# Kernel optimization log

Hardware: AMD Instinct MI355X
Metric: run time of the kernel (lower is better)

## Reference

```python
import jax, jax.numpy as jnp
import numpy as np

NUM_ENT = 50000
DIM = 128
NUM_REL = 1000  # num_rel * 2 (inverse relations)
E = 300000
SLOPE = 0.2      # args.leaky_relu_w
BN_EPS = 1e-5


def _leaky(x):
    return jax.nn.leaky_relu(x, SLOPE)


def _l2norm(x):
    n = jnp.linalg.norm(x, axis=-1, keepdims=True)
    return x / jnp.maximum(n, 1e-12)


def _batchnorm(x):
    # BatchNorm1d, training mode, fresh gamma=1/beta=0
    m = x.mean(axis=0)
    v = x.var(axis=0)
    return (x - m) / jnp.sqrt(v + BN_EPS)


def _propagate(i, j, etype, rel, x, watt, aatt, gcn, norm, num_ent):
    # gather -> relation-aware transform (opn='mult') -> attention -> scatter-add
    trans = x[j] * rel[etype]                       # [E, D]
    comb = jnp.concatenate([x[i], trans], axis=1)   # [E, 2D]
    score = (_leaky(comb @ watt) @ aatt)[:, 0]      # [E]
    # scatter softmax of attention score over destination nodes
    m = jax.ops.segment_max(score, i, num_segments=num_ent)
    m = jnp.where(jnp.isfinite(m), m, 0.0)
    e = jnp.exp(score - m[i])
    s = jax.ops.segment_sum(e, i, num_segments=num_ent)
    alpha = e / (s[i] + 1e-16)
    msg = (trans @ gcn) * alpha[:, None]
    if norm is not None:
        msg = msg * norm[:, None]
    return jax.ops.segment_sum(msg, i, num_segments=num_ent)


def _conv(ent, rel_in, edge_index, edge_type, w1, w2, gcn, loop_rel, watt, aatt):
    # RelationalAwareLayer.forward
    num_ent = ent.shape[0]
    rel = jnp.concatenate([rel_in, loop_rel], axis=0)
    rel = _leaky(rel @ w1) @ w2
    row, col = edge_index[0], edge_index[1]
    deg = jax.ops.segment_sum(jnp.ones((row.shape[0],), jnp.float32), row, num_segments=num_ent)
    dinv = jnp.where(deg > 0, deg ** -0.5, 0.0)
    norm = dinv[row]
    msg_n = _propagate(row, col, edge_type, rel, ent, watt, aatt, gcn, norm, num_ent)
    idx = jnp.arange(num_ent)
    loop_t = jnp.full((num_ent,), rel.shape[0] - 1)
    msg_s = _propagate(idx, idx, loop_t, rel, ent, watt, aatt, gcn, None, num_ent)
    return jnp.tanh(_batchnorm((msg_n + msg_s) / 2.0))


def setup_inputs() -> dict:
    key = jax.random.key(0)
    ks = jax.random.split(key, 24)
    g = lambda k, s: jax.random.normal(k, s, dtype=jnp.float32) * 0.05
    return {
        'edge_index': jax.random.randint(ks[0], (2, E), 0, NUM_ENT),
        'edge_type': jax.random.randint(ks[1], (E,), 0, NUM_REL),
        'ent_info_att': g(ks[2], (NUM_ENT, DIM)),
        'ent_completion_att': g(ks[3], (NUM_ENT, DIM)),
        'rel_completion_att': g(ks[4], (NUM_REL, DIM)),
        'rel_info_att': g(ks[5], (NUM_REL, DIM)),
        'align_linear1_1': g(ks[6], (2 * DIM, DIM)),
        'align_linear1_2': g(ks[7], (DIM, DIM)),
        'align_linear2_1': g(ks[8], (2 * DIM, DIM)),
        'align_linear2_2': g(ks[9], (DIM, DIM)),
        'rel_linear11': g(ks[10], (DIM, DIM)),
        'rel_linear12': g(ks[11], (DIM, DIM)),
        'rel_linear11_align': g(ks[12], (DIM, DIM)),
        'rel_linear12_align': g(ks[13], (DIM, DIM)),
        'all_linear_comp': g(ks[14], (3 * DIM, DIM)),
        # stacked per-layer conv params: [conv1_align, conv1_completion, conv2_align]
        'conv_w1': g(ks[15], (3, DIM, DIM)),
        'conv_w2': g(ks[16], (3, DIM, DIM)),
        'conv_gcn': g(ks[17], (3, DIM, DIM)),
        'conv_loop': g(ks[18], (3, 1, DIM)),
        'conv_watt': g(ks[19], (3, 2 * DIM, DIM)),
        'conv_aatt': g(ks[20], (3, DIM, 1)),
    }


def reference(edge_index, edge_type, ent_info_att, ent_completion_att,
              rel_completion_att, rel_info_att,
              align_linear1_1, align_linear1_2, align_linear2_1, align_linear2_2,
              rel_linear11, rel_linear12, rel_linear11_align, rel_linear12_align,
              all_linear_comp, conv_w1, conv_w2, conv_gcn, conv_loop, conv_watt, conv_aatt):
    # forward_base with num_gcn_layer == 2, dropout rate 0 (identity)
    init_comp = _l2norm(ent_completion_att)
    e1 = _leaky(jnp.concatenate([init_comp, ent_info_att], axis=1) @ align_linear1_1) @ align_linear1_2
    ao1 = _conv(e1, rel_info_att, edge_index, edge_type,
                conv_w1[0], conv_w2[0], conv_gcn[0], conv_loop[0], conv_watt[0], conv_aatt[0])
    co1 = _conv(ent_completion_att, rel_completion_att, edge_index, edge_type,
                conv_w1[1], conv_w2[1], conv_gcn[1], conv_loop[1], conv_watt[1], conv_aatt[1])
    pos1n = _l2norm(co1)
    e2 = _leaky(jnp.concatenate([pos1n, ao1], axis=1) @ align_linear2_1) @ align_linear2_2
    pr1 = _leaky(rel_completion_att @ rel_linear11) @ rel_linear12
    ari = _leaky(rel_info_att @ rel_linear11_align) @ rel_linear12_align
    ao2 = _conv(e2, ari, edge_index, edge_type,
                conv_w1[2], conv_w2[2], conv_gcn[2], conv_loop[2], conv_watt[2], conv_aatt[2])
    out = jnp.concatenate([e1, ao1, ao2], axis=1) @ all_linear_comp
    return (out, co1, pr1)
```

## Files before the change

### kernel.cpp

```cpp
#include <hip/hip_runtime.h>
#include <hip/hip_bf16.h>
#include <math.h>

#define D 128
#define DD 16384
#define NEMAX 96
typedef unsigned short u16;
typedef __attribute__((ext_vector_type(8))) short short8v;
typedef __attribute__((ext_vector_type(4))) short short4v;
typedef __attribute__((ext_vector_type(4))) float f32x4;

__device__ __forceinline__ u16 f2s(float v){
    union { __hip_bfloat16 h; u16 u; } c; c.h = __float2bfloat16(v); return c.u;
}
__device__ __forceinline__ float s2f(u16 u){
    union { __hip_bfloat16 h; u16 u; } c; c.u = u; return __bfloat162float(c.h);
}
__device__ __forceinline__ float lrelu(float x){ return x > 0.f ? x : 0.2f*x; }

__global__ void k_prepz(int* __restrict__ zz, int zw, int* __restrict__ nstart,
                        int* __restrict__ nend, int nb){
    int i = blockIdx.x*blockDim.x + threadIdx.x;
    int stride = gridDim.x*blockDim.x;
    for (int k = i; k < zw; k += stride) zz[k] = 0;
    for (int k = i; k < nb; k += stride){ nstart[k] = 0x7fffffff; nend[k] = -1; }
}
__global__ void k_f2b4(const float* __restrict__ in, u16* __restrict__ out, int n4){
    for (int i = blockIdx.x*blockDim.x + threadIdx.x; i < n4; i += gridDim.x*blockDim.x){
        float4 a = ((const float4*)in)[i];
        short4v pk;
        pk[0] = (short)f2s(a.x); pk[1] = (short)f2s(a.y);
        pk[2] = (short)f2s(a.z); pk[3] = (short)f2s(a.w);
        *(short4v*)(out + (size_t)i*4) = pk;
    }
}
__global__ void k_ideg(const int* __restrict__ row, int* __restrict__ deg, int E_){
    for (int i = blockIdx.x*blockDim.x + threadIdx.x; i < E_; i += gridDim.x*blockDim.x)
        atomicAdd(&deg[row[i]], 1);
}
__global__ void k_scan1(const int* __restrict__ ideg, int* __restrict__ rowptr,
                        int* __restrict__ bsum, int n){
    __shared__ int buf[256];
    int t = threadIdx.x, i = blockIdx.x*256 + t;
    int v = (i < n) ? ideg[i] : 0;
    buf[t] = v;
    __syncthreads();
    #pragma unroll
    for (int o = 1; o < 256; o <<= 1){
        int u = (t >= o) ? buf[t-o] : 0;
        __syncthreads();
        buf[t] += u;
        __syncthreads();
    }
    if (i < n) rowptr[i] = buf[t] - v;
    if (t == 255) bsum[blockIdx.x] = buf[255];
}
__global__ void k_scan2(int* __restrict__ bsum, int nb){
    __shared__ int buf[256];
    __shared__ int carry_s;
    int t = threadIdx.x;
    if (t == 0) carry_s = 0;
    __syncthreads();
    for (int base = 0; base < nb; base += 256){
        int v = (base + t < nb) ? bsum[base + t] : 0;
        buf[t] = v;
        __syncthreads();
        #pragma unroll
        for (int o = 1; o < 256; o <<= 1){
            int u = (t >= o) ? buf[t-o] : 0;
            __syncthreads();
            buf[t] += u;
            __syncthreads();
        }
        if (base + t < nb) bsum[base + t] = carry_s + buf[t] - v;
        int last = buf[255];
        __syncthreads();
        if (t == 0) carry_s += last;
        __syncthreads();
    }
}
__global__ void k_scan3(int* __restrict__ rowptr, const int* __restrict__ bsum,
                        int n, int E_){
    int i = blockIdx.x*blockDim.x + threadIdx.x;
    if (i < n) rowptr[i] += bsum[i >> 8];
    if (i == 0) rowptr[n] = E_;
}
__global__ void k_scatter(const int* __restrict__ row, const int* __restrict__ rowptr,
                          int* __restrict__ cnt, int* __restrict__ perm, int E_){
    for (int e = blockIdx.x*blockDim.x + threadIdx.x; e < E_; e += gridDim.x*blockDim.x){
        int i = row[e];
        int pos = rowptr[i] + atomicAdd(&cnt[i], 1);
        perm[pos] = e;
    }
}
__global__ void k_bmap(const int* __restrict__ rowptr, int* __restrict__ nstart,
                       int* __restrict__ nend, int n){
    for (int i = blockIdx.x*blockDim.x + threadIdx.x; i < n; i += gridDim.x*blockDim.x){
        int s = rowptr[i], e = rowptr[i+1];
        if (e > s){
            int b = s >> 6;
            atomicMin(&nstart[b], i);
            atomicMax(&nend[b], i);
        }
    }
}
__global__ void k_bnapply(const u16* __restrict__ acc, const float* __restrict__ gp,
                          float inv_ne, int n, u16* __restrict__ dstb,
                          float* __restrict__ dstf){
    int d = threadIdx.x & 127;
    float m = gp[d] * inv_ne;
    float var = gp[128 + d] * inv_ne - m*m;
    float sc = rsqrtf(var + 1e-5f);
    for (int i = blockIdx.x*blockDim.x + threadIdx.x; i < n; i += gridDim.x*blockDim.x){
        float v = s2f(acc[i]) * 0.5f;
        float r = tanhf((v - m) * sc);
        dstb[i] = f2s(r);
        if (dstf) dstf[i] = r;
    }
}
__global__ void k_bnapply2(const u16* __restrict__ acc0, const float* __restrict__ gp0,
                           u16* __restrict__ d0b,
                           const u16* __restrict__ acc1, const float* __restrict__ gp1,
                           u16* __restrict__ d1b, float* __restrict__ d1f,
                           float inv_ne, int n, int gb){
    int pb = blockIdx.x >= gb;
    const u16* acc = pb ? acc1 : acc0;
    const float* gp = pb ? gp1 : gp0;
    u16* db = pb ? d1b : d0b;
    float* df = pb ? d1f : nullptr;
    int b = blockIdx.x - (pb ? gb : 0);
    int d = threadIdx.x & 127;
    float m = gp[d] * inv_ne;
    float var = gp[128 + d] * inv_ne - m*m;
    float sc = rsqrtf(var + 1e-5f);
    for (int i = b*blockDim.x + threadIdx.x; i < n; i += gb*blockDim.x){
        float v = s2f(acc[i]) * 0.5f;
        float r = tanhf((v - m) * sc);
        db[i] = f2s(r);
        if (df) df[i] = r;
    }
}

__global__ void k_relprep(const float* __restrict__ rel_comp, const float* __restrict__ rel_info,
        const float* __restrict__ rl11, const float* __restrict__ rl12,
        const float* __restrict__ rl11a, const float* __restrict__ rl12a,
        const float* __restrict__ cloop, const float* __restrict__ cw1,
        const float* __restrict__ cw2, float* __restrict__ pr1out,
        float* __restrict__ rel2all, int NR){
    int b = blockIdx.x, t = threadIdx.x;
    __shared__ float v[D];
    __shared__ float h[D];
    if (b < NR){
        v[t] = rel_comp[(size_t)b*D + t];
        __syncthreads();
        float a = 0.f;
        #pragma unroll 8
        for (int k = 0; k < D; k++) a += v[k] * rl11[(size_t)k*D + t];
        h[t] = lrelu(a);
        __syncthreads();
        float o = 0.f;
        #pragma unroll 8
        for (int k = 0; k < D; k++) o += h[k] * rl12[(size_t)k*D + t];
        pr1out[(size_t)b*D + t] = o;
        return;
    }
    int bb = b - NR;
    int l = bb / (NR+1), r = bb - l*(NR+1);
    float xv;
    if (r == NR)      xv = cloop[l*D + t];
    else if (l == 1)  xv = rel_comp[(size_t)r*D + t];
    else              xv = rel_info[(size_t)r*D + t];
    v[t] = xv;
    __syncthreads();
    if (l == 2 && r < NR){
        float a = 0.f;
        #pragma unroll 8
        for (int k = 0; k < D; k++) a += v[k] * rl11a[(size_t)k*D + t];
        h[t] = lrelu(a);
        __syncthreads();
        float o = 0.f;
        #pragma unroll 8
        for (int k = 0; k < D; k++) o += h[k] * rl12a[(size_t)k*D + t];
        v[t] = o;
        __syncthreads();
    }
    const float* w1 = cw1 + (size_t)l*DD;
    const float* w2 = cw2 + (size_t)l*DD;
    float a = 0.f;
    #pragma unroll 8
    for (int k = 0; k < D; k++) a += v[k] * w1[(size_t)k*D + t];
    h[t] = lrelu(a);
    __syncthreads();
    float o = 0.f;
    #pragma unroll 8
    for (int k = 0; k < D; k++) o += h[k] * w2[(size_t)k*D + t];
    rel2all[((size_t)l*(NR+1) + r)*D + t] = o;
}

struct TEnt { const float* s; u16* d; int ldd; };
struct TTab { TEnt e[18]; };
__global__ void k_wprep(TTab tab){
    TEnt en = tab.e[blockIdx.x];
    int t = threadIdx.x;
    int n = t >> 1, h = t & 1;
    #pragma unroll
    for (int g = 0; g < 8; ++g){
        int k0 = h*64 + g*8;
        short8v pk;
        #pragma unroll
        for (int q = 0; q < 8; ++q) pk[q] = (short)f2s(en.s[(size_t)(k0+q)*D + n]);
        *(short8v*)(en.d + (size_t)n*en.ldd + k0) = pk;
    }
}

struct Srcs { const void* p0; const void* p1; const void* p2; int f0, f1, f2; };

template<int NSEG, int EPI, bool RSN>
__global__ __launch_bounds__(256) void k_mrow(Srcs S, const u16* __restrict__ WT,
        void* __restrict__ out, int NE_){
    __shared__ __align__(16) short As[128*128];
    int tid = threadIdx.x;
    int row0 = blockIdx.x * 128;
    int lane = tid & 63, w = tid >> 6;
    int l15 = lane & 15, lq = lane >> 4;
    int nhalf = w & 1, mquad = w >> 1;
    f32x4 acc[4][4];
    #pragma unroll
    for (int a = 0; a < 4; a++)
        #pragma unroll
        for (int b = 0; b < 4; b++) acc[a][b] = (f32x4){0.f,0.f,0.f,0.f};

    int sr = tid >> 1, sh = tid & 1;
    int rr = row0 + sr; if (rr >= NE_) rr = NE_ - 1;

    #pragma unroll
    for (int s = 0; s < NSEG; ++s){
        const void* sp = (s == 0) ? S.p0 : (s == 1) ? S.p1 : S.p2;
        int sf = (s == 0) ? S.f0 : (s == 1) ? S.f1 : S.f2;
        if (s) __syncthreads();
        #pragma unroll
        for (int g = 0; g < 8; ++g){
            int k8 = sh*64 + g*8;
            short8v pk;
            if (sf){
                const float* fp = (const float*)sp + (size_t)rr*D + k8;
                #pragma unroll
                for (int q = 0; q < 8; ++q) pk[q] = (short)f2s(fp[q]);
            } else {
                pk = *(const short8v*)((const u16*)sp + (size_t)rr*D + k8);
            }
            *(short8v*)(As + sr*D + (((k8>>3) ^ (sr&7))<<3)) = pk;
        }
        if (RSN && s == 0){
            float ss = 0.f;
            #pragma unroll
            for (int g = 0; g < 8; ++g){
                int k8 = sh*64 + g*8;
                short8v v = *(const short8v*)(As + sr*D + (((k8>>3) ^ (sr&7))<<3));
                #pragma unroll
                for (int q = 0; q < 8; ++q){ float f = s2f((u16)v[q]); ss += f*f; }
            }
            ss += __shfl_xor(ss, 1, 64);
            float rsc = 1.f / fmaxf(sqrtf(ss), 1e-12f);
            #pragma unroll
            for (int g = 0; g < 8; ++g){
                int k8 = sh*64 + g*8;
                short* ap = As + sr*D + (((k8>>3) ^ (sr&7))<<3);
                short8v v = *(const short8v*)ap;
                short8v pk;
                #pragma unroll
                for (int q = 0; q < 8; ++q) pk[q] = (short)f2s(s2f((u16)v[q]) * rsc);
                *(short8v*)ap = pk;
            }
        }
        __syncthreads();
        short8v bfr[4][4];
        #pragma unroll
        for (int nt = 0; nt < 4; ++nt)
            #pragma unroll
            for (int kk = 0; kk < 4; ++kk){
                size_t idx = (size_t)(nhalf*64 + nt*16 + l15)*(NSEG*D) + (size_t)s*D + kk*32 + lq*8;
                bfr[nt][kk] = *(const short8v*)(WT + idx);
            }
        #pragma unroll
        for (int mt = 0; mt < 4; ++mt){
            int ar = mquad*64 + mt*16 + l15;
            short8v afr[4];
            #pragma unroll
            for (int kk = 0; kk < 4; ++kk)
                afr[kk] = *(const short8v*)(As + ar*D + (((kk*4 + lq) ^ (ar&7))<<3));
            #pragma unroll
            for (int nt = 0; nt < 4; ++nt)
                #pragma unroll
                for (int kk = 0; kk < 4; ++kk)
                    acc[mt][nt] = __builtin_amdgcn_mfma_f32_16x16x32_bf16(
                        afr[kk], bfr[nt][kk], acc[mt][nt], 0, 0, 0);
        }
    }
    #pragma unroll
    for (int mt = 0; mt < 4; ++mt){
        #pragma unroll
        for (int nt = 0; nt < 4; ++nt){
            #pragma unroll
            for (int r = 0; r < 4; ++r){
                int gr = row0 + mquad*64 + mt*16 + lq*4 + r;
                if (gr >= NE_) continue;
                int c = nhalf*64 + nt*16 + l15;
                float v = acc[mt][nt][r];
                if (EPI == 0) ((float*)out)[(size_t)gr*D + c] = v;
                else ((u16*)out)[(size_t)gr*D + c] = f2s(EPI == 2 ? lrelu(v) : v);
            }
        }
    }
}

struct ConvP { const u16* x; const u16* WT; u16* out; u16* ub; const float* loop; float* gp; };

template<int MODE>
__global__ __launch_bounds__(256) void k_mrow2(ConvP A, ConvP B, int rb, int NE_){
    __shared__ __align__(16) short As[128*128];
    int pb = blockIdx.x >= rb;
    ConvP P = pb ? B : A;
    int row0 = (blockIdx.x - (pb ? rb : 0)) * 128;
    int tid = threadIdx.x;
    int lane = tid & 63, w = tid >> 6;
    int l15 = lane & 15, lq = lane >> 4;
    int nhalf = w & 1, mquad = w >> 1;
    f32x4 acc[4][4];
    #pragma unroll
    for (int a = 0; a < 4; a++)
        #pragma unroll
        for (int b = 0; b < 4; b++) acc[a][b] = (f32x4){0.f,0.f,0.f,0.f};

    int sr = tid >> 1, sh = tid & 1;
    int rr = row0 + sr; if (rr >= NE_) rr = NE_ - 1;
    #pragma unroll
    for (int g = 0; g < 8; ++g){
        int k8 = sh*64 + g*8;
        short8v pk = *(const short8v*)(P.x + (size_t)rr*D + k8);
        *(short8v*)(As + sr*D + (((k8>>3) ^ (sr&7))<<3)) = pk;
    }
    __syncthreads();
    short8v bfr[4][4];
    #pragma unroll
    for (int nt = 0; nt < 4; ++nt)
        #pragma unroll
        for (int kk = 0; kk < 4; ++kk)
            bfr[nt][kk] = *(const short8v*)(P.WT + (size_t)(nhalf*64 + nt*16 + l15)*D + kk*32 + lq*8);
    #pragma unroll
    for (int mt = 0; mt < 4; ++mt){
        int ar = mquad*64 + mt*16 + l15;
        short8v afr[4];
        #pragma unroll
        for (int kk = 0; kk < 4; ++kk)
            afr[kk] = *(const short8v*)(As + ar*D + (((kk*4 + lq) ^ (ar&7))<<3));
        #pragma unroll
        for (int nt = 0; nt < 4; ++nt)
            #pragma unroll
            for (int kk = 0; kk < 4; ++kk)
                acc[mt][nt] = __builtin_amdgcn_mfma_f32_16x16x32_bf16(
                    afr[kk], bfr[nt][kk], acc[mt][nt], 0, 0, 0);
    }
    if (MODE == 3){
        float cs[4] = {0,0,0,0}, cs2[4] = {0,0,0,0};
        #pragma unroll
        for (int mt = 0; mt < 4; ++mt)
            #pragma unroll
            for (int nt = 0; nt < 4; ++nt)
                #pragma unroll
                for (int r = 0; r < 4; ++r){
                    int gr = row0 + mquad*64 + mt*16 + lq*4 + r;
                    if (gr >= NE_) continue;
                    int c = nhalf*64 + nt*16 + l15;
                    float v = acc[mt][nt][r];
                    P.out[(size_t)gr*D + c] = f2s(v);
                    float h = v * 0.5f;
                    cs[nt] += h; cs2[nt] += h*h;
                }
        __syncthreads();
        float* ps  = (float*)As;
        float* ps2 = ps + 1024;
        int slot = mquad*4 + lq;
        #pragma unroll
        for (int nt = 0; nt < 4; ++nt){
            int c = nhalf*64 + nt*16 + l15;
            ps[slot*128 + c]  = cs[nt];
            ps2[slot*128 + c] = cs2[nt];
        }
        __syncthreads();
        if (tid < 128){
            float s = 0.f, s2 = 0.f;
            #pragma unroll
            for (int q = 0; q < 8; ++q){ s += ps[q*128 + tid]; s2 += ps2[q*128 + tid]; }
            atomicAdd(&P.gp[tid], s);
            atomicAdd(&P.gp[128 + tid], s2);
        }
    } else {
        #pragma unroll
        for (int mt = 0; mt < 4; ++mt)
            #pragma unroll
            for (int nt = 0; nt < 4; ++nt)
                #pragma unroll
                for (int r = 0; r < 4; ++r){
                    int gr = row0 + mquad*64 + mt*16 + lq*4 + r;
                    if (gr >= NE_) continue;
                    int c = nhalf*64 + nt*16 + l15;
                    P.out[(size_t)gr*D + c] = f2s(acc[mt][nt][r]);
                }
        for (int idx = tid; idx < 128*128; idx += 256){
            int r2 = idx >> 7, c = idx & 127;
            int gr = row0 + r2;
            if (gr < NE_){
                float v = s2f((u16)As[r2*D + ((((c>>3) ^ (r2&7))<<3) | (c&7))]) * P.loop[c];
                P.ub[(size_t)gr*D + c] = f2s(v);
            }
        }
    }
}

struct FP { const u16* x; const float* rel2; const u16* xattb; const u16* WT;
            const float* aatt; const float* loop; u16* u; };

__global__ __launch_bounds__(256) void k_fedge(
        const int* __restrict__ coli, const int* __restrict__ ety,
        const int* __restrict__ rowptr, const int* __restrict__ perm,
        const int* __restrict__ nstart, const int* __restrict__ nend,
        FP fa, FP fb, int nb){
    __shared__ __align__(16) short As[NEMAX*D];
    __shared__ u16 jL[NEMAX], kL[NEMAX], iL[NEMAX];
    __shared__ float sc[NEMAX];
    __shared__ float red[2][NEMAX];
    int pb = blockIdx.x >= nb;
    FP P = pb ? fb : fa;
    int b = blockIdx.x - (pb ? nb : 0);
    int ns = nstart[b];
    if (ns == 0x7fffffff) return;
    int nn = nend[b] - ns + 1;
    int tid = threadIdx.x;
    int estart = rowptr[ns];
    int ne = rowptr[ns + nn] - estart;
    if (ne > NEMAX) ne = NEMAX;
    int T = (ne + 15) >> 4;
    int nrows = T << 4;
    if (tid < ne){
        int e = perm[estart + tid];
        jL[tid] = (u16)coli[e]; kL[tid] = (u16)ety[e];
    }
    if (tid < nn){
        int i = ns + tid;
        int s0 = rowptr[i] - estart, s1 = rowptr[i+1] - estart;
        if (s0 < 0) s0 = 0;
        if (s1 > NEMAX) s1 = NEMAX;
        for (int p = s0; p < s1; ++p) iL[p] = (u16)i;
    }
    __syncthreads();
    for (int it = tid; it < nrows*4; it += 256){
        int p = it >> 2, part = it & 3;
        int ps = (p < ne) ? p : (ne - 1);
        int j = jL[ps], krel = kL[ps];
        #pragma unroll
        for (int g = 0; g < 4; ++g){
            int k8 = part*32 + g*8;
            short8v sv = *(const short8v*)(P.x + (size_t)j*D + k8);
            const float* rp = P.rel2 + (size_t)krel*D + k8;
            short8v pk;
            #pragma unroll
            for (int q = 0; q < 8; ++q) pk[q] = (short)f2s(s2f((u16)sv[q]) * rp[q]);
            *(short8v*)(As + p*D + (((k8>>3) ^ (p&7))<<3)) = pk;
        }
    }
    __syncthreads();
    int lane = tid & 63, w = tid >> 6;
    int l15 = lane & 15, lq = lane >> 4;
    int nhalf = w & 1, mq = w >> 1;
    short8v bfr[4][4];
    #pragma unroll
    for (int nt = 0; nt < 4; ++nt)
        #pragma unroll
        for (int kk = 0; kk < 4; ++kk)
            bfr[nt][kk] = *(const short8v*)(P.WT + (size_t)(nhalf*64 + nt*16 + l15)*D + kk*32 + lq*8);
    float av[4];
    #pragma unroll
    for (int nt = 0; nt < 4; ++nt) av[nt] = P.aatt[nhalf*64 + nt*16 + l15];

    for (int t = mq; t < T; t += 2){
        float xv[4][4];
        #pragma unroll
        for (int r = 0; r < 4; ++r){
            int el = t*16 + lq*4 + r;
            int ep = (el < ne) ? el : (ne - 1);
            int ii = iL[ep];
            #pragma unroll
            for (int nt = 0; nt < 4; ++nt)
                xv[r][nt] = s2f(P.xattb[(size_t)ii*D + nhalf*64 + nt*16 + l15]);
        }
        int ar = t*16 + l15;
        short8v afr[4];
        #pragma unroll
        for (int kk = 0; kk < 4; ++kk)
            afr[kk] = *(const short8v*)(As + ar*D + (((kk*4 + lq) ^ (ar&7))<<3));
        f32x4 acc[4];
        #pragma unroll
        for (int nt = 0; nt < 4; ++nt) acc[nt] = (f32x4){0.f,0.f,0.f,0.f};
        #pragma unroll
        for (int nt = 0; nt < 4; ++nt)
            #pragma unroll
            for (int kk = 0; kk < 4; ++kk)
                acc[nt] = __builtin_amdgcn_mfma_f32_16x16x32_bf16(
                    afr[kk], bfr[nt][kk], acc[nt], 0, 0, 0);
        #pragma unroll
        for (int r = 0; r < 4; ++r){
            int el = t*16 + lq*4 + r;
            float p = 0.f;
            if (el < ne){
                #pragma unroll
                for (int nt = 0; nt < 4; ++nt)
                    p += lrelu(acc[nt][r] + xv[r][nt]) * av[nt];
            }
            p += __shfl_xor(p, 1, 64);
            p += __shfl_xor(p, 2, 64);
            p += __shfl_xor(p, 4, 64);
            p += __shfl_xor(p, 8, 64);
            if (l15 == 0 && el < NEMAX) red[nhalf][el] = p;
        }
    }
    __syncthreads();
    if (tid < ne) sc[tid] = expf(red[0][tid] + red[1][tid]);
    __syncthreads();
    if (tid < nn){
        int i = ns + tid;
        int s0 = rowptr[i] - estart, s1 = rowptr[i+1] - estart;
        if (s1 > NEMAX) s1 = NEMAX;
        if (s1 > s0){
            float sum = 0.f;
            for (int p = s0; p < s1; ++p) sum += sc[p];
            float coef = rsqrtf((float)(s1 - s0)) / (sum + 1e-16f);
            for (int p = s0; p < s1; ++p) sc[p] *= coef;
        }
    }
    __syncthreads();
    int c = tid & 127, nh = tid >> 7;
    float loopc = P.loop[c];
    for (int n0 = nh; n0 < nn; n0 += 16){
        float xi[8];
        int cnt = 0;
        for (int n = n0; n < nn && cnt < 8; n += 2, ++cnt)
            xi[cnt] = s2f(P.x[(size_t)(ns + n)*D + c]);
        cnt = 0;
        for (int n = n0; n < nn && cnt < 8; n += 2, ++cnt){
            int i = ns + n;
            int s0 = rowptr[i] - estart, s1 = rowptr[i+1] - estart;
            if (s1 > NEMAX) s1 = NEMAX;
            if (s1 <= s0) continue;
            float a = xi[cnt] * loopc;
            int p = s0;
            for (; p + 4 <= s1; p += 4){
                float v0 = s2f((u16)As[(p+0)*D + ((((c>>3) ^ ((p+0)&7))<<3) | (c&7))]);
                float v1 = s2f((u16)As[(p+1)*D + ((((c>>3) ^ ((p+1)&7))<<3) | (c&7))]);
                float v2 = s2f((u16)As[(p+2)*D + ((((c>>3) ^ ((p+2)&7))<<3) | (c&7))]);
                float v3 = s2f((u16)As[(p+3)*D + ((((c>>3) ^ ((p+3)&7))<<3) | (c&7))]);
                a += sc[p]*v0 + sc[p+1]*v1 + sc[p+2]*v2 + sc[p+3]*v3;
            }
            for (; p < s1; ++p)
                a += sc[p] * s2f((u16)As[p*D + ((((c>>3) ^ (p&7))<<3) | (c&7))]);
            P.u[(size_t)i*D + c] = f2s(a);
        }
    }
}

extern "C" void kernel_launch(void* const* d_in, const int* in_sizes, int n_in,
                              void* d_out, int out_size, void* d_ws, size_t ws_size,
                              hipStream_t stream){
    const int* eidx = (const int*)d_in[0];
    const int* ety  = (const int*)d_in[1];
    const float* ent_info = (const float*)d_in[2];
    const float* ent_comp = (const float*)d_in[3];
    const float* rel_comp = (const float*)d_in[4];
    const float* rel_info = (const float*)d_in[5];
    const float* al11 = (const float*)d_in[6],  *al12 = (const float*)d_in[7];
    const float* al21 = (const float*)d_in[8],  *al22 = (const float*)d_in[9];
    const float* rl11 = (const float*)d_in[10], *rl12 = (const float*)d_in[11];
    const float* rl11a = (const float*)d_in[12], *rl12a = (const float*)d_in[13];
    const float* allw = (const float*)d_in[14];
    const float* cw1 = (const float*)d_in[15], *cw2 = (const float*)d_in[16];
    const float* cgcn = (const float*)d_in[17], *cloop = (const float*)d_in[18];
    const float* cwatt = (const float*)d_in[19], *caatt = (const float*)d_in[20];

    const int E  = in_sizes[1];
    const int NE = in_sizes[2] / D;
    const int NR = in_sizes[4] / D;
    const int* row = eidx;
    const int* col = eidx + E;
    const size_t NEd = (size_t)NE * D;
    float* outp = (float*)d_out;
    const int NB64 = (E + 63) / 64;

    char* wsb = (char*)d_ws;
    size_t off = 0;
    auto takeB = [&](size_t bytes) -> void* {
        void* q = wsb + off;
        off = (off + bytes + 255) & ~(size_t)255;
        return q;
    };
    u16*   slotA = (u16*) takeB(NEd * 2);
    u16*   hb    = slotA;
    u16*   accB0 = slotA;
    u16*   xattb0= (u16*) takeB(NEd * 2);
    u16*   ub0   = (u16*) takeB(NEd * 2);
    u16*   e1b   = (u16*) takeB(NEd * 2);
    u16*   ao1b  = (u16*) takeB(NEd * 2);
    u16*   e2b   = (u16*) takeB(NEd * 2);
    u16*   cob   = (u16*) takeB(NEd * 2);
    float* rel2all = (float*)takeB((size_t)3*(NR+1)*D*4);
    int*   rowptr= (int*)  takeB((size_t)(NE+1)*4);
    int*   perm  = (int*)  takeB((size_t)E*4);
    int*   bsum  = (int*)  takeB(1024*4);
    int*   nstart= (int*)  takeB((size_t)NB64*4);
    int*   nend  = (int*)  takeB((size_t)NB64*4);
    int ZW = 2*NE + 768;
    int*   zz    = (int*)  takeB((size_t)ZW*4);
    int*   ideg  = zz;
    int*   cnt   = zz + NE;
    float* gp3   = (float*)(zz + 2*NE);
    u16*   wtXatt = (u16*)takeB((size_t)3*DD*2);
    u16*   wtScore= (u16*)takeB((size_t)3*DD*2);
    u16*   wtGcn  = (u16*)takeB((size_t)3*DD*2);
    u16*   wtAl11 = (u16*)takeB((size_t)2*DD*2);
    u16*   wtAl12 = (u16*)takeB((size_t)DD*2);
    u16*   wtAl21 = (u16*)takeB((size_t)2*DD*2);
    u16*   wtAl22 = (u16*)takeB((size_t)DD*2);
    u16*   wtAllw = (u16*)takeB((size_t)3*DD*2);
    u16*   xcb   = e2b;

    size_t slab = ((NEd*2 + 255) & ~(size_t)255);
    bool wide = (off + 3*slab) <= ws_size;
    u16* xattb1 = wide ? (u16*)takeB(NEd * 2) : xattb0;
    u16* ub1    = wide ? (u16*)takeB(NEd * 2) : ub0;
    u16* accB1  = wide ? (u16*)takeB(NEd * 2) : accB0;

    const int GS = 2048, BS = 256;
    const int RB = (NE + 127) / 128;
    const int NB = (NE + 255) / 256;
    const float inv_ne = 1.f / (float)NE;

    TTab tab;
    int ti = 0;
    for (int l = 0; l < 3; ++l){
        tab.e[ti++] = { cwatt + (size_t)l*2*DD,        wtXatt  + (size_t)l*DD, 128 };
        tab.e[ti++] = { cwatt + (size_t)l*2*DD + DD,   wtScore + (size_t)l*DD, 128 };
        tab.e[ti++] = { cgcn  + (size_t)l*DD,          wtGcn   + (size_t)l*DD, 128 };
    }
    tab.e[ti++] = { al11,       wtAl11,        256 };
    tab.e[ti++] = { al11 + DD,  wtAl11 + 128,  256 };
    tab.e[ti++] = { al12,       wtAl12,        128 };
    tab.e[ti++] = { al21,       wtAl21,        256 };
    tab.e[ti++] = { al21 + DD,  wtAl21 + 128,  256 };
    tab.e[ti++] = { al22,       wtAl22,        128 };
    tab.e[ti++] = { allw,            wtAllw,        384 };
    tab.e[ti++] = { allw + DD,       wtAllw + 128,  384 };
    tab.e[ti++] = { allw + 2*DD,     wtAllw + 256,  384 };
    k_wprep<<<18, 256, 0, stream>>>(tab);

    k_prepz<<<256, BS, 0, stream>>>(zz, ZW, nstart, nend, NB64);
    k_f2b4<<<GS, BS, 0, stream>>>(ent_comp, xcb, (int)(NEd/4));
    k_ideg<<<GS, BS, 0, stream>>>(row, ideg, E);
    k_scan1<<<NB, 256, 0, stream>>>(ideg, rowptr, bsum, NE);
    k_scan2<<<1, 256, 0, stream>>>(bsum, NB);
    k_scan3<<<NB, 256, 0, stream>>>(rowptr, bsum, NE, E);
    k_scatter<<<GS, BS, 0, stream>>>(row, rowptr, cnt, perm, E);
    k_bmap<<<NB, 256, 0, stream>>>(rowptr, nstart, nend, NE);

    k_relprep<<<NR + 3*(NR+1), D, 0, stream>>>(rel_comp, rel_info, rl11, rl12,
                                               rl11a, rl12a, cloop, cw1, cw2,
                                               outp + 2*NEd, rel2all, NR);

    {
        Srcs S{ ent_comp, ent_info, nullptr, 1, 1, 0 };
        k_mrow<2, 2, true><<<RB, 256, 0, stream>>>(S, wtAl11, hb, NE);
        Srcs S2{ hb, nullptr, nullptr, 0, 0, 0 };
        k_mrow<1, 1, false><<<RB, 256, 0, stream>>>(S2, wtAl12, e1b, NE);
    }

    auto conv_seq = [&](const u16* x, int l, u16* xab, u16* ubp, u16* acb,
                        u16* dstb, float* dstf){
        const float* rel2l = rel2all + (size_t)l*(NR+1)*D;
        float* gp = gp3 + (size_t)l*256;
        ConvP A4{ x, wtXatt + (size_t)l*DD, xab, ubp, rel2l + (size_t)NR*D, nullptr };
        k_mrow2<4><<<RB, 256, 0, stream>>>(A4, A4, RB, NE);
        FP fa{ x, rel2l, xab, wtScore + (size_t)l*DD, caatt + (size_t)l*D,
               rel2l + (size_t)NR*D, ubp };
        k_fedge<<<NB64, 256, 0, stream>>>(col, ety, rowptr, perm, nstart, nend,
                                          fa, fa, NB64);
        ConvP A3{ ubp, wtGcn + (size_t)l*DD, acb, nullptr, nullptr, gp };
        k_mrow2<3><<<RB, 256, 0, stream>>>(A3, A3, RB, NE);
        k_bnapply<<<GS, BS, 0, stream>>>(acb, gp, inv_ne, (int)NEd, dstb, dstf);
    };

    if (wide){
        const float* rel2_0 = rel2all;
        const float* rel2_1 = rel2all + (size_t)(NR+1)*D;
        ConvP A4{ e1b, wtXatt,      xattb0, ub0, rel2_0 + (size_t)NR*D, nullptr };
        ConvP B4{ xcb, wtXatt + DD, xattb1, ub1, rel2_1 + (size_t)NR*D, nullptr };
        k_mrow2<4><<<2*RB, 256, 0, stream>>>(A4, B4, RB, NE);
        FP fa{ e1b, rel2_0, xattb0, wtScore,      caatt,     rel2_0 + (size_t)NR*D, ub0 };
        FP fb{ xcb, rel2_1, xattb1, wtScore + DD, caatt + D, rel2_1 + (size_t)NR*D, ub1 };
        k_fedge<<<2*NB64, 256, 0, stream>>>(col, ety, rowptr, perm, nstart, nend,
                                            fa, fb, NB64);
        ConvP A3{ ub0, wtGcn,      accB0, nullptr, nullptr, gp3 };
        ConvP B3{ ub1, wtGcn + DD, accB1, nullptr, nullptr, gp3 + 256 };
        k_mrow2<3><<<2*RB, 256, 0, stream>>>(A3, B3, RB, NE);
        k_bnapply2<<<2*GS, BS, 0, stream>>>(accB0, gp3, ao1b,
                                            accB1, gp3 + 256, cob, outp + NEd,
                                            inv_ne, (int)NEd, GS);
    } else {
        conv_seq(e1b, 0, xattb0, ub0, accB0, ao1b, nullptr);
        conv_seq(xcb, 1, xattb0, ub0, accB0, cob, outp + NEd);
    }

    {
        Srcs S{ cob, ao1b, nullptr, 0, 0, 0 };
        k_mrow<2, 2, true><<<RB, 256, 0, stream>>>(S, wtAl21, hb, NE);
        Srcs S2{ hb, nullptr, nullptr, 0, 0, 0 };
        k_mrow<1, 1, false><<<RB, 256, 0, stream>>>(S2, wtAl22, e2b, NE);
    }

    conv_seq(e2b, 2, xattb0, ub0, accB0, cob, nullptr);

    {
        Srcs S{ e1b, ao1b, cob, 0, 0, 0 };
        k_mrow<3, 0, false><<<RB, 256, 0, stream>>>(S, wtAllw, outp, NE);
    }
}
```

Measured before the change: 685.7 us.

## Pack col/etype into sorted edge array and fold block map into scan

The scatter kernel now writes a packed (col, etype) word per sorted edge position instead of a permutation index, so the edge kernel reads one contiguous array rather than doing indirect gathers through perm into col and ety. The k_bmap kernel is removed and its node-to-block min/max bookkeeping moves into k_scan3 using ideg, which drops one launch. The final per-node aggregation loop in k_fedge is simplified by removing the x prefetch batching. Packing assumes col fits in 16 bits, which the earlier u16 casts already assumed.

```diff
diff --git a/kernel.cpp b/kernel.cpp
--- a/kernel.cpp
+++ b/kernel.cpp
@@ -80,28 +80,27 @@
     }
 }
 __global__ void k_scan3(int* __restrict__ rowptr, const int* __restrict__ bsum,
-                        int n, int E_){
+                        const int* __restrict__ ideg, int* __restrict__ nstart,
+                        int* __restrict__ nend, int n, int E_){
     int i = blockIdx.x*blockDim.x + threadIdx.x;
-    if (i < n) rowptr[i] += bsum[i >> 8];
-    if (i == 0) rowptr[n] = E_;
-}
-__global__ void k_scatter(const int* __restrict__ row, const int* __restrict__ rowptr,
-                          int* __restrict__ cnt, int* __restrict__ perm, int E_){
+    if (i < n){
+        int rpi = rowptr[i] + bsum[i >> 8];
+        rowptr[i] = rpi;
+        if (i == 0) rowptr[n] = E_;
+        if (ideg[i] > 0){
+            int b = rpi >> 6;
+            atomicMin(&nstart[b], i);
+            atomicMax(&nend[b], i);
+        }
+    }
+}
+__global__ void k_scatter(const int* __restrict__ row, const int* __restrict__ col,
+                          const int* __restrict__ ety, const int* __restrict__ rowptr,
+                          int* __restrict__ cnt, unsigned* __restrict__ jk, int E_){
     for (int e = blockIdx.x*blockDim.x + threadIdx.x; e < E_; e += gridDim.x*blockDim.x){
         int i = row[e];
         int pos = rowptr[i] + atomicAdd(&cnt[i], 1);
-        perm[pos] = e;
-    }
-}
-__global__ void k_bmap(const int* __restrict__ rowptr, int* __restrict__ nstart,
-                       int* __restrict__ nend, int n){
-    for (int i = blockIdx.x*blockDim.x + threadIdx.x; i < n; i += gridDim.x*blockDim.x){
-        int s = rowptr[i], e = rowptr[i+1];
-        if (e > s){
-            int b = s >> 6;
-            atomicMin(&nstart[b], i);
-            atomicMax(&nend[b], i);
-        }
+        jk[pos] = ((unsigned)col[e] & 0xFFFFu) | ((unsigned)ety[e] << 16);
     }
 }
 __global__ void k_bnapply(const u16* __restrict__ acc, const float* __restrict__ gp,
@@ -422,8 +421,8 @@
             const float* aatt; const float* loop; u16* u; };
 
 __global__ __launch_bounds__(256) void k_fedge(
-        const int* __restrict__ coli, const int* __restrict__ ety,
-        const int* __restrict__ rowptr, const int* __restrict__ perm,
+        const unsigned* __restrict__ jk,
+        const int* __restrict__ rowptr,
         const int* __restrict__ nstart, const int* __restrict__ nend,
         FP fa, FP fb, int nb){
     __shared__ __align__(16) short As[NEMAX*D];
@@ -443,8 +442,8 @@
     int T = (ne + 15) >> 4;
     int nrows = T << 4;
     if (tid < ne){
-        int e = perm[estart + tid];
-        jL[tid] = (u16)coli[e]; kL[tid] = (u16)ety[e];
+        unsigned v = jk[estart + tid];
+        jL[tid] = (u16)(v & 0xFFFFu); kL[tid] = (u16)(v >> 16);
     }
     if (tid < nn){
         int i = ns + tid;
@@ -541,30 +540,23 @@
     __syncthreads();
     int c = tid & 127, nh = tid >> 7;
     float loopc = P.loop[c];
-    for (int n0 = nh; n0 < nn; n0 += 16){
-        float xi[8];
-        int cnt = 0;
-        for (int n = n0; n < nn && cnt < 8; n += 2, ++cnt)
-            xi[cnt] = s2f(P.x[(size_t)(ns + n)*D + c]);
-        cnt = 0;
-        for (int n = n0; n < nn && cnt < 8; n += 2, ++cnt){
-            int i = ns + n;
-            int s0 = rowptr[i] - estart, s1 = rowptr[i+1] - estart;
-            if (s1 > NEMAX) s1 = NEMAX;
-            if (s1 <= s0) continue;
-            float a = xi[cnt] * loopc;
-            int p = s0;
-            for (; p + 4 <= s1; p += 4){
-                float v0 = s2f((u16)As[(p+0)*D + ((((c>>3) ^ ((p+0)&7))<<3) | (c&7))]);
-                float v1 = s2f((u16)As[(p+1)*D + ((((c>>3) ^ ((p+1)&7))<<3) | (c&7))]);
-                float v2 = s2f((u16)As[(p+2)*D + ((((c>>3) ^ ((p+2)&7))<<3) | (c&7))]);
-                float v3 = s2f((u16)As[(p+3)*D + ((((c>>3) ^ ((p+3)&7))<<3) | (c&7))]);
-                a += sc[p]*v0 + sc[p+1]*v1 + sc[p+2]*v2 + sc[p+3]*v3;
-            }
-            for (; p < s1; ++p)
-                a += sc[p] * s2f((u16)As[p*D + ((((c>>3) ^ (p&7))<<3) | (c&7))]);
-            P.u[(size_t)i*D + c] = f2s(a);
-        }
+    for (int n = nh; n < nn; n += 2){
+        int i = ns + n;
+        int s0 = rowptr[i] - estart, s1 = rowptr[i+1] - estart;
+        if (s1 > NEMAX) s1 = NEMAX;
+        if (s1 <= s0) continue;
+        float a = s2f(P.x[(size_t)i*D + c]) * loopc;
+        int p = s0;
+        for (; p + 4 <= s1; p += 4){
+            float v0 = s2f((u16)As[(p+0)*D + ((((c>>3) ^ ((p+0)&7))<<3) | (c&7))]);
+            float v1 = s2f((u16)As[(p+1)*D + ((((c>>3) ^ ((p+1)&7))<<3) | (c&7))]);
+            float v2 = s2f((u16)As[(p+2)*D + ((((c>>3) ^ ((p+2)&7))<<3) | (c&7))]);
+            float v3 = s2f((u16)As[(p+3)*D + ((((c>>3) ^ ((p+3)&7))<<3) | (c&7))]);
+            a += sc[p]*v0 + sc[p+1]*v1 + sc[p+2]*v2 + sc[p+3]*v3;
+        }
+        for (; p < s1; ++p)
+            a += sc[p] * s2f((u16)As[p*D + ((((c>>3) ^ (p&7))<<3) | (c&7))]);
+        P.u[(size_t)i*D + c] = f2s(a);
     }
 }
 
@@ -613,7 +605,7 @@
     u16*   cob   = (u16*) takeB(NEd * 2);
     float* rel2all = (float*)takeB((size_t)3*(NR+1)*D*4);
     int*   rowptr= (int*)  takeB((size_t)(NE+1)*4);
-    int*   perm  = (int*)  takeB((size_t)E*4);
+    unsigned* jk = (unsigned*)takeB((size_t)E*4);
     int*   bsum  = (int*)  takeB(1024*4);
     int*   nstart= (int*)  takeB((size_t)NB64*4);
     int*   nend  = (int*)  takeB((size_t)NB64*4);
@@ -666,9 +658,8 @@
     k_ideg<<<GS, BS, 0, stream>>>(row, ideg, E);
     k_scan1<<<NB, 256, 0, stream>>>(ideg, rowptr, bsum, NE);
     k_scan2<<<1, 256, 0, stream>>>(bsum, NB);
-    k_scan3<<<NB, 256, 0, stream>>>(rowptr, bsum, NE, E);
-    k_scatter<<<GS, BS, 0, stream>>>(row, rowptr, cnt, perm, E);
-    k_bmap<<<NB, 256, 0, stream>>>(rowptr, nstart, nend, NE);
+    k_scan3<<<NB, 256, 0, stream>>>(rowptr, bsum, ideg, nstart, nend, NE, E);
+    k_scatter<<<GS, BS, 0, stream>>>(row, col, ety, rowptr, cnt, jk, E);
 
     k_relprep<<<NR + 3*(NR+1), D, 0, stream>>>(rel_comp, rel_info, rl11, rl12,
                                                rl11a, rl12a, cloop, cw1, cw2,
@@ -689,8 +680,7 @@
         k_mrow2<4><<<RB, 256, 0, stream>>>(A4, A4, RB, NE);
         FP fa{ x, rel2l, xab, wtScore + (size_t)l*DD, caatt + (size_t)l*D,
                rel2l + (size_t)NR*D, ubp };
-        k_fedge<<<NB64, 256, 0, stream>>>(col, ety, rowptr, perm, nstart, nend,
-                                          fa, fa, NB64);
+        k_fedge<<<NB64, 256, 0, stream>>>(jk, rowptr, nstart, nend, fa, fa, NB64);
         ConvP A3{ ubp, wtGcn + (size_t)l*DD, acb, nullptr, nullptr, gp };
         k_mrow2<3><<<RB, 256, 0, stream>>>(A3, A3, RB, NE);
         k_bnapply<<<GS, BS, 0, stream>>>(acb, gp, inv_ne, (int)NEd, dstb, dstf);
@@ -704,8 +694,7 @@
         k_mrow2<4><<<2*RB, 256, 0, stream>>>(A4, B4, RB, NE);
         FP fa{ e1b, rel2_0, xattb0, wtScore,      caatt,     rel2_0 + (size_t)NR*D, ub0 };
         FP fb{ xcb, rel2_1, xattb1, wtScore + DD, caatt + D, rel2_1 + (size_t)NR*D, ub1 };
-        k_fedge<<<2*NB64, 256, 0, stream>>>(col, ety, rowptr, perm, nstart, nend,
-                                            fa, fb, NB64);
+        k_fedge<<<2*NB64, 256, 0, stream>>>(jk, rowptr, nstart, nend, fa, fb, NB64);
         ConvP A3{ ub0, wtGcn,      accB0, nullptr, nullptr, gp3 };
         ConvP B3{ ub1, wtGcn + DD, accB1, nullptr, nullptr, gp3 + 256 };
         k_mrow2<3><<<2*RB, 256, 0, stream>>>(A3, B3, RB, NE);
```

Result: faster. 664.4 us (median of 2 runs) (-3.1%).
